# Kernel optimization log

Measured on AMD Instinct MI355X. Metric: run time of the kernel, lower is better.

The kernel has to match this reference:

```python
import jax, jax.numpy as jnp
import numpy as np

N, E, F_IN, H, C = 50000, 800000, 128, 64, 10

def setup_inputs() -> dict:
    key = jax.random.key(0)
    ks = jax.random.split(key, 8)
    x = jax.random.normal(ks[0], (N, F_IN), dtype=jnp.float32)
    edge_index = jax.random.randint(ks[1], (2, E), 0, N, dtype=jnp.int32)
    edge_weight = jax.random.uniform(ks[2], (E,), dtype=jnp.float32)
    W1 = jax.random.normal(ks[3], (H, F_IN), dtype=jnp.float32) * 0.05
    W2 = jax.random.normal(ks[4], (H, H), dtype=jnp.float32) * 0.05
    W3 = jax.random.normal(ks[5], (C, H), dtype=jnp.float32) * 0.05
    b1 = jnp.zeros((H,), jnp.float32)
    b2 = jnp.zeros((H,), jnp.float32)
    b3 = jnp.zeros((C,), jnp.float32)
    return {"x": x, "edge_index": edge_index, "edge_weight": edge_weight,
            "W1": W1, "b1": b1, "W2": W2, "b2": b2, "W3": W3, "b3": b3}

def reference(x, edge_index, edge_weight, W1, b1, W2, b2, W3, b3):
    n = x.shape[0]
    row, col = edge_index[0], edge_index[1]
    # GCN symmetric normalization (add_self_loops=False): deg from edge weights on col
    deg = jax.ops.segment_sum(edge_weight, col, num_segments=n)  # [N]
    dinv = jnp.where(deg > 0, jax.lax.rsqrt(deg), 0.0)
    norm = dinv[row] * edge_weight * dinv[col]  # [E]

    def gcn_layer(h, W, b):
        h = h @ W.T                               # linear transform [N, out]
        msg = h[row] * norm[:, None]              # gather + scale   [E, out]
        agg = jax.ops.segment_sum(msg, col, num_segments=n)  # scatter-add [N, out]
        return agg + b

    h = gcn_layer(x, W1, b1)
    h = gcn_layer(h, W2, b2)
    logits = gcn_layer(h, W3, b3)
    soft = jax.nn.softmax(logits, axis=1)
    return logits, soft
```

## Files before the change

### kernel.cpp

```cpp
#include <hip/hip_runtime.h>
#include <hip/hip_fp16.h>

#define N_NODES 50000
#define N_EDGES 800000
#define F_IN    128
#define H_DIM   64
#define C_DIM   10
#define CPAD    16
#define CAP     48
#define BLOCK   256
#define QN      64
#define NSUB    ((N_NODES + QN - 1) / QN)
#define SSTRIDE 1280
#define E_BLK   2048
#define ABLOCKS ((N_EDGES + E_BLK - 1) / E_BLK)
#define GBLK    2048
#define NWAVES  (GBLK * 4)
#define POISON  ((int)0xAAAAAAAA)

__device__ __forceinline__ int unbase(int v) {
    return ((unsigned)v < 65536u) ? v : v - POISON;
}

__device__ __forceinline__ int   prow(unsigned v) { return (int)(v >> 16); }
__device__ __forceinline__ float pw(unsigned v)   {
    return __half2float(__ushort_as_half((unsigned short)(v & 0xFFFFu)));
}

__global__ __launch_bounds__(256) void k_binA(const int* __restrict__ rows,
                                              const int* __restrict__ cols,
                                              const float* __restrict__ ew,
                                              const float* __restrict__ W1,
                                              const float* __restrict__ b1,
                                              const float* __restrict__ W2,
                                              const float* __restrict__ b2,
                                              const float* __restrict__ W3,
                                              int* __restrict__ bucketCnt,
                                              unsigned* __restrict__ regionA,
                                              unsigned short* __restrict__ regionC,
                                              float* __restrict__ T2g,
                                              float* __restrict__ v1g,
                                              float* __restrict__ v2g) {
    const int tid = threadIdx.x;
    if (blockIdx.x < ABLOCKS) {
        __shared__ unsigned       sA[E_BLK];
        __shared__ unsigned short sC[E_BLK];
        __shared__ int hcnt[NSUB];
        __shared__ int lbase[NSUB];
        __shared__ int gb[NSUB];
        __shared__ int wtot[4];
        for (int i = tid; i < NSUB; i += BLOCK) hcnt[i] = 0;
        __syncthreads();

        const int e0 = blockIdx.x * E_BLK;
        unsigned rw[8];
        unsigned cl[8];
#pragma unroll
        for (int j = 0; j < 8; ++j) {
            int e = e0 + j * BLOCK + tid;
            if (e < N_EDGES) {
                int   c = cols[e];
                int   r = rows[e];
                float w = ew[e];
                rw[j] = ((unsigned)r << 16) | (unsigned)__half_as_ushort(__float2half(w));
                int lr = atomicAdd(&hcnt[c >> 6], 1);
                cl[j] = (unsigned)c | ((unsigned)lr << 16);
            } else {
                cl[j] = 0xFFFFFFFFu;
            }
        }
        __syncthreads();

        const int lane = tid & 63, wid = tid >> 6;
        const int b4 = tid << 2;
        int h0 = (b4 + 0 < NSUB) ? hcnt[b4 + 0] : 0;
        int h1 = (b4 + 1 < NSUB) ? hcnt[b4 + 1] : 0;
        int h2 = (b4 + 2 < NSUB) ? hcnt[b4 + 2] : 0;
        int h3 = (b4 + 3 < NSUB) ? hcnt[b4 + 3] : 0;
        int ls = h0 + h1 + h2 + h3;
        int incl = ls;
#pragma unroll
        for (int off = 1; off < 64; off <<= 1) {
            int t = __shfl_up(incl, off);
            if (lane >= off) incl += t;
        }
        if (lane == 63) wtot[wid] = incl;
        __syncthreads();
        int woff = 0;
#pragma unroll
        for (int w = 0; w < 4; ++w) if (w < wid) woff += wtot[w];
        int run = woff + incl - ls;
        if (b4 + 0 < NSUB) { lbase[b4 + 0] = run; run += h0; }
        if (b4 + 1 < NSUB) { lbase[b4 + 1] = run; run += h1; }
        if (b4 + 2 < NSUB) { lbase[b4 + 2] = run; run += h2; }
        if (b4 + 3 < NSUB) { lbase[b4 + 3] = run; run += h3; }
        const int total = wtot[0] + wtot[1] + wtot[2] + wtot[3];
        __syncthreads();

#pragma unroll
        for (int j = 0; j < 8; ++j) {
            if (cl[j] != 0xFFFFFFFFu) {
                int c  = (int)(cl[j] & 0xFFFFu);
                int lr = (int)(cl[j] >> 16);
                int pos = lbase[c >> 6] + lr;
                sA[pos] = rw[j];
                sC[pos] = (unsigned short)c;
            }
        }
        for (int i = tid; i < NSUB; i += BLOCK)
            if (hcnt[i] > 0) gb[i] = unbase(atomicAdd(&bucketCnt[i], hcnt[i]));
        __syncthreads();

        for (int i = tid; i < total; i += BLOCK) {
            int c = sC[i];
            int s = c >> 6;
            int gpos = gb[s] + (i - lbase[s]);
            if (gpos < SSTRIDE) {
                size_t p = (size_t)s * SSTRIDE + gpos;
                regionA[p] = sA[i];
                regionC[p] = (unsigned short)c;
            }
        }
        return;
    }

    __shared__ float u[C_DIM * H_DIM];
    for (int idx = tid; idx < C_DIM * H_DIM; idx += BLOCK) {
        int c = idx >> 6, j = idx & 63;
        float a = 0.f;
#pragma unroll
        for (int k = 0; k < H_DIM; ++k) a += W3[c * H_DIM + k] * W2[k * H_DIM + j];
        u[idx] = a;
    }
    __syncthreads();
    for (int idx = tid; idx < C_DIM * F_IN; idx += BLOCK) {
        int c = idx >> 7, f = idx & 127;
        float a = 0.f;
#pragma unroll
        for (int k = 0; k < H_DIM; ++k) a += u[c * H_DIM + k] * W1[k * F_IN + f];
        T2g[idx] = a;
    }
    if (tid < C_DIM) {
        float a = 0.f, b = 0.f;
#pragma unroll
        for (int k = 0; k < H_DIM; ++k) {
            a += u[tid * H_DIM + k] * b1[k];
            b += W3[tid * H_DIM + k] * b2[k];
        }
        v1g[tid] = a;
        v2g[tid] = b;
    }
}

__global__ __launch_bounds__(256) void k_binB(const int* __restrict__ bucketCnt,
                                              const unsigned* __restrict__ regionA,
                                              const unsigned short* __restrict__ regionC,
                                              const float* __restrict__ x,
                                              const float* __restrict__ T2g,
                                              float2* __restrict__ meta,
                                              unsigned* __restrict__ edata,
                                              __half* __restrict__ bufA) {
    __shared__ unsigned sdata[QN * CAP];
    __shared__ int   lcnt[QN];
    __shared__ float wsum[QN];
    __shared__ float dinvs[QN];
    __shared__ float ts[16 * 132];
    __shared__ float xs[16][132];
    const int tid = threadIdx.x;
    const int s   = blockIdx.x;
    const int n0  = s * QN;
    if (n0 >= N_NODES) return;
    if (tid < QN) { lcnt[tid] = 0; wsum[tid] = 0.f; }
    for (int i = tid; i < 16 * F_IN; i += BLOCK) {
        int c = i >> 7;
        ts[c * 132 + (i & 127)] = (c < C_DIM) ? T2g[i] : 0.f;
    }
    __syncthreads();

    int tot = unbase(bucketCnt[s]);
    if (tot > SSTRIDE) tot = SSTRIDE;
    const size_t segBase = (size_t)s * SSTRIDE;
    for (int i = tid; i < tot; i += BLOCK) {
        unsigned e = regionA[segBase + i];
        int nl = (int)regionC[segBase + i] & (QN - 1);
        int r = atomicAdd(&lcnt[nl], 1);
        if (r < CAP) sdata[nl * CAP + r] = e;
        atomicAdd(&wsum[nl], pw(e));
    }
    __syncthreads();

    const int nvalid = min(N_NODES - n0, QN);
    if (tid < nvalid) {
        int c0 = min(lcnt[tid], CAP);
        int cp = (c0 + 15) & ~15;
        if (cp > CAP) cp = CAP;
        for (int r = c0; r < cp; ++r) sdata[tid * CAP + r] = 0u;
        float d = wsum[tid];
        float di = d > 0.f ? rsqrtf(d) : 0.f;
        dinvs[tid] = di;
        meta[n0 + tid] = make_float2(di, (float)cp);
    }
    __syncthreads();

    {
        int4* dst = reinterpret_cast<int4*>(edata + (size_t)n0 * CAP);
        const int4* src = reinterpret_cast<const int4*>(sdata);
        const int nvec = nvalid * (CAP / 4);
        for (int i = tid; i < nvec; i += BLOCK) dst[i] = src[i];
    }

    const int g = tid >> 4, c = tid & 15;
    for (int t = 0; t < QN / 16; ++t) {
        __syncthreads();
        const int n0t = n0 + t * 16;
        for (int i = tid; i < 16 * 32; i += BLOCK) {
            int ln = i >> 5, f4 = i & 31;
            if (n0t + ln < N_NODES) {
                float4 v = reinterpret_cast<const float4*>(x)[(n0t + ln) * 32 + f4];
                *reinterpret_cast<float4*>(&xs[ln][f4 * 4]) = v;
            }
        }
        __syncthreads();
        const int n = n0t + g;
        if (n < N_NODES) {
            const float di = dinvs[t * 16 + g];
            const float4* tsv = reinterpret_cast<const float4*>(&ts[c * 132]);
            const float4* xv  = reinterpret_cast<const float4*>(&xs[g][0]);
            float a = 0.f;
#pragma unroll 8
            for (int f4 = 0; f4 < 32; ++f4) {
                float4 xx = xv[f4], tt = tsv[f4];
                a += xx.x * tt.x + xx.y * tt.y + xx.z * tt.z + xx.w * tt.w;
            }
            float outv = (c < C_DIM) ? a * di : (c == 10 ? di : 0.f);
            bufA[n * CPAD + c] = __float2half(outv);
        }
    }
}

__global__ __launch_bounds__(256) void k_gather(const float2* __restrict__ meta,
                                                const unsigned* __restrict__ edata,
                                                const __half* __restrict__ zin,
                                                __half* __restrict__ zout) {
    const int lane = threadIdx.x & 63;
    const int sub = lane >> 3;
    const int c2  = lane & 7;
    const int w0 = (blockIdx.x * 256 + threadIdx.x) >> 6;
    for (int n = w0; n < N_NODES; n += NWAVES) {
        float2 m = meta[n];
        const float di = m.x;
        const int iters = ((int)m.y) >> 4;
        const uint2* bp = reinterpret_cast<const uint2*>(edata + n * CAP) + sub;
        float ax = 0.f, ay = 0.f;
#pragma unroll
        for (int i = 0; i < 3; ++i) {
            if (i < iters) {
                uint2 e = bp[i * 8];
                {
                    float2 z = __half22float2(
                        reinterpret_cast<const __half2*>(zin + prow(e.x) * CPAD)[c2]);
                    float w = pw(e.x);
                    ax += w * z.x; ay += w * z.y;
                }
                {
                    float2 z = __half22float2(
                        reinterpret_cast<const __half2*>(zin + prow(e.y) * CPAD)[c2]);
                    float w = pw(e.y);
                    ax += w * z.x; ay += w * z.y;
                }
            }
        }
        ax += __shfl_xor(ax, 8);  ay += __shfl_xor(ay, 8);
        ax += __shfl_xor(ax, 16); ay += __shfl_xor(ay, 16);
        ax += __shfl_xor(ax, 32); ay += __shfl_xor(ay, 32);
        if (lane < 8) {
            float sc = di * di;
            reinterpret_cast<__half2*>(zout + n * CPAD)[lane] =
                __floats2half2_rn(ax * sc, ay * sc);
        }
    }
}

__global__ __launch_bounds__(256) void k_final(const float2* __restrict__ meta,
                                               const unsigned* __restrict__ edata,
                                               const __half* __restrict__ zin,
                                               const __half* __restrict__ s1buf,
                                               const float* __restrict__ v1,
                                               const float* __restrict__ v2,
                                               const float* __restrict__ b3,
                                               float* __restrict__ logits,
                                               float* __restrict__ soft) {
    const int lane = threadIdx.x & 63;
    const int sub = lane >> 3;
    const int c2  = lane & 7;
    const int w0 = (blockIdx.x * 256 + threadIdx.x) >> 6;
    for (int n = w0; n < N_NODES; n += NWAVES) {
        float2 m = meta[n];
        const float di = m.x;
        const int iters = ((int)m.y) >> 4;
        const uint2* bp = reinterpret_cast<const uint2*>(edata + n * CAP) + sub;
        float ax = 0.f, ay = 0.f;
#pragma unroll
        for (int i = 0; i < 3; ++i) {
            if (i < iters) {
                uint2 e = bp[i * 8];
                {
                    float2 z = __half22float2(
                        reinterpret_cast<const __half2*>(zin + prow(e.x) * CPAD)[c2]);
                    float w = pw(e.x);
                    ax += w * z.x; ay += w * z.y;
                }
                {
                    float2 z = __half22float2(
                        reinterpret_cast<const __half2*>(zin + prow(e.y) * CPAD)[c2]);
                    float w = pw(e.y);
                    ax += w * z.x; ay += w * z.y;
                }
            }
        }
        ax += __shfl_xor(ax, 8);  ay += __shfl_xor(ay, 8);
        ax += __shfl_xor(ax, 16); ay += __shfl_xor(ay, 16);
        ax += __shfl_xor(ax, 32); ay += __shfl_xor(ay, 32);

        const float r  = di > 0.f ? 1.0f / di : 0.f;
        const float a1 = __half2float(s1buf[n * CPAD + 10]) * r;
        const float a2 = __half2float(zin[n * CPAD + 10]) * r;
        float l0 = -1e30f, l1 = -1e30f;
        if (c2 < 5) {
            float2 w1 = reinterpret_cast<const float2*>(v1)[c2];
            float2 w2 = reinterpret_cast<const float2*>(v2)[c2];
            float2 bb = reinterpret_cast<const float2*>(b3)[c2];
            l0 = di * ax + a2 * w1.x + a1 * w2.x + bb.x;
            l1 = di * ay + a2 * w1.y + a1 * w2.y + bb.y;
        }
        float mx = fmaxf(l0, l1);
        mx = fmaxf(mx, __shfl_xor(mx, 1));
        mx = fmaxf(mx, __shfl_xor(mx, 2));
        mx = fmaxf(mx, __shfl_xor(mx, 4));
        float e0 = (c2 < 5) ? __expf(l0 - mx) : 0.f;
        float e1 = (c2 < 5) ? __expf(l1 - mx) : 0.f;
        float ss = e0 + e1;
        ss += __shfl_xor(ss, 1);
        ss += __shfl_xor(ss, 2);
        ss += __shfl_xor(ss, 4);
        if (lane < 5) {
            float inv = 1.0f / ss;
            reinterpret_cast<float2*>(logits + (size_t)n * C_DIM)[lane] = make_float2(l0, l1);
            reinterpret_cast<float2*>(soft   + (size_t)n * C_DIM)[lane] = make_float2(e0 * inv, e1 * inv);
        }
    }
}

extern "C" void kernel_launch(void* const* d_in, const int* in_sizes, int n_in,
                              void* d_out, int out_size, void* d_ws, size_t ws_size,
                              hipStream_t stream) {
    const float* x  = (const float*)d_in[0];
    const int*   ei = (const int*)d_in[1];
    const float* ew = (const float*)d_in[2];
    const float* W1 = (const float*)d_in[3];
    const float* b1 = (const float*)d_in[4];
    const float* W2 = (const float*)d_in[5];
    const float* b2 = (const float*)d_in[6];
    const float* W3 = (const float*)d_in[7];
    const float* b3 = (const float*)d_in[8];
    const int* rows = ei;
    const int* cols = ei + N_EDGES;

    char* ws = (char*)d_ws;
    size_t off = 0;
    auto alloc = [&](size_t bytes) { void* q = ws + off; off += (bytes + 15) & ~size_t(15); return q; };

    float2*         meta      = (float2*)         alloc((size_t)N_NODES * 8);
    __half*         bufA      = (__half*)         alloc((size_t)N_NODES * CPAD * 2);
    __half*         bufB      = (__half*)         alloc((size_t)N_NODES * CPAD * 2);
    float*          T2g       = (float*)          alloc(C_DIM * F_IN * 4);
    float*          v1        = (float*)          alloc(64);
    float*          v2        = (float*)          alloc(64);
    int*            bucketCnt = (int*)            alloc(NSUB * 4);
    unsigned*       regionA   = (unsigned*)       alloc((size_t)NSUB * SSTRIDE * 4);
    unsigned short* regionC   = (unsigned short*) alloc((size_t)NSUB * SSTRIDE * 2);
    unsigned*       edata     = (unsigned*)       alloc((size_t)N_NODES * CAP * 4);

    float* logits = (float*)d_out;
    float* soft   = logits + N_NODES * C_DIM;

    k_binA<<<ABLOCKS + 1, BLOCK, 0, stream>>>(rows, cols, ew, W1, b1, W2, b2, W3,
                                              bucketCnt, regionA, regionC, T2g, v1, v2);
    k_binB<<<NSUB, BLOCK, 0, stream>>>(bucketCnt, regionA, regionC, x, T2g,
                                       meta, edata, bufA);
    k_gather<<<GBLK, BLOCK, 0, stream>>>(meta, edata, bufA, bufB);
    k_gather<<<GBLK, BLOCK, 0, stream>>>(meta, edata, bufB, bufA);
    k_final<<<GBLK, BLOCK, 0, stream>>>(meta, edata, bufA, bufB, v1, v2, b3,
                                        logits, soft);
}
```

Before: 163.7 us.

## Batch seven nodes per wave in gather kernels with full-CAP unconditional edge loads

The gather and final kernels now give each wave a fixed block of seven consecutive nodes instead of a grid-stride loop. All edge words for those nodes are loaded up front and then gathered without a per-node trip-count branch, so more independent memory requests are in flight at once. To make the fixed trip count valid, the bucketing stage pads every node's edge list with zeros out to CAP. Each node now always processes 48 slots, which adds wasted gathers of row 0 for padding, and each thread holds more registers.

```diff
diff --git a/kernel.cpp b/kernel.cpp
--- a/kernel.cpp
+++ b/kernel.cpp
@@ -16,6 +16,7 @@
 #define ABLOCKS ((N_EDGES + E_BLK - 1) / E_BLK)
 #define GBLK    2048
 #define NWAVES  (GBLK * 4)
+#define NPW     7
 #define POISON  ((int)0xAAAAAAAA)
 
 __device__ __forceinline__ int unbase(int v) {
@@ -192,13 +193,11 @@
     const int nvalid = min(N_NODES - n0, QN);
     if (tid < nvalid) {
         int c0 = min(lcnt[tid], CAP);
-        int cp = (c0 + 15) & ~15;
-        if (cp > CAP) cp = CAP;
-        for (int r = c0; r < cp; ++r) sdata[tid * CAP + r] = 0u;
+        for (int r = c0; r < CAP; ++r) sdata[tid * CAP + r] = 0u;
         float d = wsum[tid];
         float di = d > 0.f ? rsqrtf(d) : 0.f;
         dinvs[tid] = di;
-        meta[n0 + tid] = make_float2(di, (float)cp);
+        meta[n0 + tid] = make_float2(di, (float)CAP);
     }
     __syncthreads();
 
@@ -245,38 +244,61 @@
     const int lane = threadIdx.x & 63;
     const int sub = lane >> 3;
     const int c2  = lane & 7;
-    const int w0 = (blockIdx.x * 256 + threadIdx.x) >> 6;
-    for (int n = w0; n < N_NODES; n += NWAVES) {
-        float2 m = meta[n];
-        const float di = m.x;
-        const int iters = ((int)m.y) >> 4;
-        const uint2* bp = reinterpret_cast<const uint2*>(edata + n * CAP) + sub;
-        float ax = 0.f, ay = 0.f;
-#pragma unroll
-        for (int i = 0; i < 3; ++i) {
-            if (i < iters) {
-                uint2 e = bp[i * 8];
-                {
-                    float2 z = __half22float2(
-                        reinterpret_cast<const __half2*>(zin + prow(e.x) * CPAD)[c2]);
-                    float w = pw(e.x);
-                    ax += w * z.x; ay += w * z.y;
-                }
-                {
-                    float2 z = __half22float2(
-                        reinterpret_cast<const __half2*>(zin + prow(e.y) * CPAD)[c2]);
-                    float w = pw(e.y);
-                    ax += w * z.x; ay += w * z.y;
-                }
-            }
-        }
-        ax += __shfl_xor(ax, 8);  ay += __shfl_xor(ay, 8);
-        ax += __shfl_xor(ax, 16); ay += __shfl_xor(ay, 16);
-        ax += __shfl_xor(ax, 32); ay += __shfl_xor(ay, 32);
+    const int w   = (blockIdx.x * 256 + threadIdx.x) >> 6;
+    const int n0  = w * NPW;
+    if (n0 >= N_NODES) return;
+
+    uint2 e[NPW][3];
+#pragma unroll
+    for (int i = 0; i < NPW; ++i) {
+        int n = n0 + i;
+        if (n < N_NODES) {
+            const uint2* bp = reinterpret_cast<const uint2*>(edata + n * CAP) + sub;
+            e[i][0] = bp[0];
+            e[i][1] = bp[8];
+            e[i][2] = bp[16];
+        } else {
+            e[i][0] = make_uint2(0u, 0u);
+            e[i][1] = make_uint2(0u, 0u);
+            e[i][2] = make_uint2(0u, 0u);
+        }
+    }
+
+    float ax[NPW], ay[NPW];
+#pragma unroll
+    for (int i = 0; i < NPW; ++i) {
+        ax[i] = 0.f; ay[i] = 0.f;
+#pragma unroll
+        for (int j = 0; j < 3; ++j) {
+            uint2 ee = e[i][j];
+            {
+                float2 z = __half22float2(
+                    reinterpret_cast<const __half2*>(zin + prow(ee.x) * CPAD)[c2]);
+                float wt = pw(ee.x);
+                ax[i] += wt * z.x; ay[i] += wt * z.y;
+            }
+            {
+                float2 z = __half22float2(
+                    reinterpret_cast<const __half2*>(zin + prow(ee.y) * CPAD)[c2]);
+                float wt = pw(ee.y);
+                ax[i] += wt * z.x; ay[i] += wt * z.y;
+            }
+        }
+    }
+
+#pragma unroll
+    for (int i = 0; i < NPW; ++i) {
+        int n = n0 + i;
+        if (n >= N_NODES) break;
+        float axx = ax[i], ayy = ay[i];
+        axx += __shfl_xor(axx, 8);  ayy += __shfl_xor(ayy, 8);
+        axx += __shfl_xor(axx, 16); ayy += __shfl_xor(ayy, 16);
+        axx += __shfl_xor(axx, 32); ayy += __shfl_xor(ayy, 32);
         if (lane < 8) {
+            float di = meta[n].x;
             float sc = di * di;
             reinterpret_cast<__half2*>(zout + n * CPAD)[lane] =
-                __floats2half2_rn(ax * sc, ay * sc);
+                __floats2half2_rn(axx * sc, ayy * sc);
         }
     }
 }
@@ -293,35 +315,58 @@
     const int lane = threadIdx.x & 63;
     const int sub = lane >> 3;
     const int c2  = lane & 7;
-    const int w0 = (blockIdx.x * 256 + threadIdx.x) >> 6;
-    for (int n = w0; n < N_NODES; n += NWAVES) {
-        float2 m = meta[n];
-        const float di = m.x;
-        const int iters = ((int)m.y) >> 4;
-        const uint2* bp = reinterpret_cast<const uint2*>(edata + n * CAP) + sub;
-        float ax = 0.f, ay = 0.f;
-#pragma unroll
-        for (int i = 0; i < 3; ++i) {
-            if (i < iters) {
-                uint2 e = bp[i * 8];
-                {
-                    float2 z = __half22float2(
-                        reinterpret_cast<const __half2*>(zin + prow(e.x) * CPAD)[c2]);
-                    float w = pw(e.x);
-                    ax += w * z.x; ay += w * z.y;
-                }
-                {
-                    float2 z = __half22float2(
-                        reinterpret_cast<const __half2*>(zin + prow(e.y) * CPAD)[c2]);
-                    float w = pw(e.y);
-                    ax += w * z.x; ay += w * z.y;
-                }
-            }
-        }
-        ax += __shfl_xor(ax, 8);  ay += __shfl_xor(ay, 8);
-        ax += __shfl_xor(ax, 16); ay += __shfl_xor(ay, 16);
-        ax += __shfl_xor(ax, 32); ay += __shfl_xor(ay, 32);
-
+    const int w   = (blockIdx.x * 256 + threadIdx.x) >> 6;
+    const int n0  = w * NPW;
+    if (n0 >= N_NODES) return;
+
+    uint2 e[NPW][3];
+#pragma unroll
+    for (int i = 0; i < NPW; ++i) {
+        int n = n0 + i;
+        if (n < N_NODES) {
+            const uint2* bp = reinterpret_cast<const uint2*>(edata + n * CAP) + sub;
+            e[i][0] = bp[0];
+            e[i][1] = bp[8];
+            e[i][2] = bp[16];
+        } else {
+            e[i][0] = make_uint2(0u, 0u);
+            e[i][1] = make_uint2(0u, 0u);
+            e[i][2] = make_uint2(0u, 0u);
+        }
+    }
+
+    float ax[NPW], ay[NPW];
+#pragma unroll
+    for (int i = 0; i < NPW; ++i) {
+        ax[i] = 0.f; ay[i] = 0.f;
+#pragma unroll
+        for (int j = 0; j < 3; ++j) {
+            uint2 ee = e[i][j];
+            {
+                float2 z = __half22float2(
+                    reinterpret_cast<const __half2*>(zin + prow(ee.x) * CPAD)[c2]);
+                float wt = pw(ee.x);
+                ax[i] += wt * z.x; ay[i] += wt * z.y;
+            }
+            {
+                float2 z = __half22float2(
+                    reinterpret_cast<const __half2*>(zin + prow(ee.y) * CPAD)[c2]);
+                float wt = pw(ee.y);
+                ax[i] += wt * z.x; ay[i] += wt * z.y;
+            }
+        }
+    }
+
+#pragma unroll
+    for (int i = 0; i < NPW; ++i) {
+        int n = n0 + i;
+        if (n >= N_NODES) break;
+        float axx = ax[i], ayy = ay[i];
+        axx += __shfl_xor(axx, 8);  ayy += __shfl_xor(ayy, 8);
+        axx += __shfl_xor(axx, 16); ayy += __shfl_xor(ayy, 16);
+        axx += __shfl_xor(axx, 32); ayy += __shfl_xor(ayy, 32);
+
+        const float di = meta[n].x;
         const float r  = di > 0.f ? 1.0f / di : 0.f;
         const float a1 = __half2float(s1buf[n * CPAD + 10]) * r;
         const float a2 = __half2float(zin[n * CPAD + 10]) * r;
@@ -330,8 +375,8 @@
             float2 w1 = reinterpret_cast<const float2*>(v1)[c2];
             float2 w2 = reinterpret_cast<const float2*>(v2)[c2];
             float2 bb = reinterpret_cast<const float2*>(b3)[c2];
-            l0 = di * ax + a2 * w1.x + a1 * w2.x + bb.x;
-            l1 = di * ay + a2 * w1.y + a1 * w2.y + bb.y;
+            l0 = di * axx + a2 * w1.x + a1 * w2.x + bb.x;
+            l1 = di * ayy + a2 * w1.y + a1 * w2.y + bb.y;
         }
         float mx = fmaxf(l0, l1);
         mx = fmaxf(mx, __shfl_xor(mx, 1));
```

Result: slower. 173.5 us (+6.0%).
